# Kernel optimization log

Hardware: AMD Instinct MI355X
Metric: run time of the kernel (lower is better)

The kernel has to match this reference:

```python
import jax, jax.numpy as jnp
import numpy as np
import math

FEAT_DIM = 128
N_BANK = 1000000
K_NEG = 4096
BATCH = 256
T = 0.5
MOMENTUM = 0.5
EPS = 1e-7


def setup_inputs() -> dict:
    key = jax.random.key(0)
    k1, k2, k3, k4, k5, k6 = jax.random.split(key, 6)
    stdv = 1.0 / math.sqrt(FEAT_DIM / 3)
    memory_l = jax.random.uniform(k1, (N_BANK, FEAT_DIM), minval=-stdv, maxval=stdv, dtype=jnp.float32)
    memory_ab = jax.random.uniform(k2, (N_BANK, FEAT_DIM), minval=-stdv, maxval=stdv, dtype=jnp.float32)
    l = jax.random.normal(k3, (BATCH, FEAT_DIM), dtype=jnp.float32)
    ab = jax.random.normal(k4, (BATCH, FEAT_DIM), dtype=jnp.float32)
    y = jax.random.randint(k5, (BATCH,), 0, N_BANK, dtype=jnp.int32)
    idx = jax.random.randint(k6, (BATCH, K_NEG + 1), 0, N_BANK, dtype=jnp.int32)
    idx = idx.at[:, 0].set(y)  # positive sample in slot 0, as in torch forward
    return {"l": l, "ab": ab, "memory_l": memory_l, "memory_ab": memory_ab, "y": y, "idx": idx}


def _l2_normalize(x):
    # matches torch: x / (sqrt(sum(x^2)) + eps)
    return x / (jnp.sqrt(jnp.sum(x * x, axis=1, keepdims=True)) + EPS)


def _momentum_update(memory, y, x_norm):
    # gather rows, momentum mix, renormalize, scatter back
    pos = memory[y] * MOMENTUM + x_norm * (1.0 - MOMENTUM)          # [B, D]
    norm = jnp.sqrt(jnp.sum(pos * pos, axis=1, keepdims=True))
    return memory.at[y].set(pos / norm)


def reference(l, ab, memory_l, memory_ab, y, idx):
    outputSize = memory_l.shape[0]
    ln = _l2_normalize(l)
    abn = _l2_normalize(ab)

    # gather negatives+positive from the AB bank, score against l features
    w_ab = jax.lax.stop_gradient(memory_ab[idx])                     # [B, K+1, D]
    P_l = jnp.exp(jnp.einsum('bkd,bd->bk', w_ab, ln) / T)[..., None]  # [B, K+1, 1]
    Z_l = jnp.mean(P_l) * outputSize
    out_l = P_l / Z_l

    w_l = jax.lax.stop_gradient(memory_l[idx])                       # [B, K+1, D]
    P_ab = jnp.exp(jnp.einsum('bkd,bd->bk', w_l, abn) / T)[..., None]
    Z_ab = jnp.mean(P_ab) * outputSize
    out_ab = P_ab / Z_ab

    # momentum scatter update of the memory banks (no_grad in torch)
    new_memory_l = jax.lax.stop_gradient(_momentum_update(memory_l, y, ln))
    new_memory_ab = jax.lax.stop_gradient(_momentum_update(memory_ab, y, abn))

    return out_l, out_ab, new_memory_l, new_memory_ab
```

## Files before the change

### kernel.cpp

```cpp
#include <hip/hip_runtime.h>
#include <math.h>
#include <stdint.h>

#define FEAT   128
#define NBANK  1000000
#define KP1    4097
#define BATCH  256
#define INV_T  2.0f
#define EPS_N  1e-7f

constexpr size_t TOTP   = (size_t)BATCH * KP1;
constexpr size_t O_OUTL = 0;
constexpr size_t O_OUTA = TOTP;
constexpr size_t O_MEML = 2 * TOTP;
constexpr size_t O_MEMA = O_MEML + (size_t)NBANK * FEAT;

constexpr int RPB   = 16;
constexpr int NBUCK = NBANK / RPB;
constexpr int CAP   = 64;

constexpr int CHUNK  = 31;
constexpr int GRID_M = (NBUCK + CHUNK - 1) / CHUNK;

constexpr size_t WS_LN   = 0;
constexpr size_t WS_ABN  = 32768;
constexpr size_t WS_PL   = 65544;
constexpr size_t WS_PA   = 65800;
constexpr size_t WS_U32  = 66560;

typedef float vfloat4 __attribute__((ext_vector_type(4)));

__device__ __forceinline__ float dot4(vfloat4 a, vfloat4 b) {
    return a.x * b.x + a.y * b.y + a.z * b.z + a.w * b.w;
}

__global__ void norm_zero_kernel(const float* __restrict__ l,
                                 const float* __restrict__ ab,
                                 float* __restrict__ ws,
                                 unsigned int* __restrict__ cnt) {
    int b    = blockIdx.x;
    int lane = threadIdx.x;
    for (int i = b * 64 + lane; i < NBUCK; i += 512 * 64) cnt[i] = 0u;
    const float* src;
    float*       dst;
    if (b < BATCH) { src = l  + (size_t)b * FEAT;            dst = ws + WS_LN  + (size_t)b * FEAT; }
    else           { src = ab + (size_t)(b - BATCH) * FEAT;  dst = ws + WS_ABN + (size_t)(b - BATCH) * FEAT; }
    float2 v = *(const float2*)(src + 2 * lane);
    float  ss = v.x * v.x + v.y * v.y;
    #pragma unroll
    for (int m = 1; m < 64; m <<= 1) ss += __shfl_xor(ss, m, 64);
    float inv = 1.0f / (sqrtf(ss) + EPS_N);
    ((float2*)dst)[lane] = make_float2(v.x * inv, v.y * inv);
}

__global__ void build_kernel(const int* __restrict__ idx,
                             unsigned int* __restrict__ cnt,
                             unsigned int* __restrict__ ent) {
    size_t stride = (size_t)gridDim.x * blockDim.x;
    for (size_t p = (size_t)blockIdx.x * blockDim.x + threadIdx.x; p < TOTP; p += stride) {
        int row = idx[p];
        int b   = (int)(p / KP1);
        int k   = (int)(p - (size_t)b * KP1);
        int bucket = row >> 4;
        unsigned int pos = atomicAdd(&cnt[bucket], 1u);
        if (pos < (unsigned int)CAP)
            ent[(size_t)bucket * CAP + pos] =
                ((unsigned int)b << 17) | ((unsigned int)k << 4) | (unsigned int)(row & 15);
    }
}

__global__ __launch_bounds__(256) void main_kernel(
        const float* __restrict__ mem_l, const float* __restrict__ mem_ab,
        const float* __restrict__ ws_f,
        const unsigned int* __restrict__ cnt,
        const unsigned int* __restrict__ ent,
        float* __restrict__ out) {
    __shared__ float ldsL[RPB * FEAT];
    __shared__ float ldsA[RPB * FEAT];
    int tid = threadIdx.x;
    int w0  = blockIdx.x * CHUNK;
    int w1  = min(w0 + CHUNK, NBUCK);
    if (w0 >= NBUCK) return;

    vfloat4* lL = (vfloat4*)ldsL;
    vfloat4* lA = (vfloat4*)ldsA;
    int g = tid >> 4, lane16 = tid & 15;

    size_t fb = (size_t)w0 * RPB * FEAT;
    vfloat4 cl0 = ((const vfloat4*)(mem_l  + fb))[tid];
    vfloat4 cl1 = ((const vfloat4*)(mem_l  + fb))[256 + tid];
    vfloat4 ca0 = ((const vfloat4*)(mem_ab + fb))[tid];
    vfloat4 ca1 = ((const vfloat4*)(mem_ab + fb))[256 + tid];
    int c = min((int)cnt[w0], CAP);

    for (int w = w0; w < w1; ++w) {
        size_t fbase = (size_t)w * RPB * FEAT;
        lL[tid] = cl0; lL[256 + tid] = cl1;
        lA[tid] = ca0; lA[256 + tid] = ca1;
        ((vfloat4*)(out + O_MEML + fbase))[tid]       = cl0;
        ((vfloat4*)(out + O_MEML + fbase))[256 + tid] = cl1;
        ((vfloat4*)(out + O_MEMA + fbase))[tid]       = ca0;
        ((vfloat4*)(out + O_MEMA + fbase))[256 + tid] = ca1;
        vfloat4 nl0, nl1, na0, na1; int cn = 0;
        if (w + 1 < w1) {
            size_t nb = (size_t)(w + 1) * RPB * FEAT;
            nl0 = ((const vfloat4*)(mem_l  + nb))[tid];
            nl1 = ((const vfloat4*)(mem_l  + nb))[256 + tid];
            na0 = ((const vfloat4*)(mem_ab + nb))[tid];
            na1 = ((const vfloat4*)(mem_ab + nb))[256 + tid];
            cn  = min((int)cnt[w + 1], CAP);
        }
        asm volatile("s_waitcnt lgkmcnt(0)" ::: "memory");
        __builtin_amdgcn_s_barrier();
        for (int i = g; i < c; i += 16) {
            unsigned int ev = ent[(size_t)w * CAP + i];
            int rloc = (int)(ev & 15u);
            int k    = (int)((ev >> 4) & 0x1FFFu);
            int b    = (int)(ev >> 17);
            const vfloat4* ra = (const vfloat4*)(ldsA + rloc * FEAT) + lane16 * 2;
            const vfloat4* rl = (const vfloat4*)(ldsL + rloc * FEAT) + lane16 * 2;
            vfloat4 wa0 = ra[0], wa1 = ra[1];
            vfloat4 wl0 = rl[0], wl1 = rl[1];
            const vfloat4* lq = (const vfloat4*)(ws_f + WS_LN  + (size_t)b * FEAT) + lane16 * 2;
            const vfloat4* aq = (const vfloat4*)(ws_f + WS_ABN + (size_t)b * FEAT) + lane16 * 2;
            vfloat4 lv0 = lq[0], lv1 = lq[1];
            vfloat4 av0 = aq[0], av1 = aq[1];
            float dlv  = dot4(wa0, lv0) + dot4(wa1, lv1);
            float dabv = dot4(wl0, av0) + dot4(wl1, av1);
            #pragma unroll
            for (int m = 1; m < 16; m <<= 1) {
                dlv  += __shfl_xor(dlv,  m, 64);
                dabv += __shfl_xor(dabv, m, 64);
            }
            if (lane16 == 0) {
                out[O_OUTL + (size_t)b * KP1 + k] = __expf(dlv  * INV_T);
                out[O_OUTA + (size_t)b * KP1 + k] = __expf(dabv * INV_T);
            }
        }
        __builtin_amdgcn_s_barrier();
        cl0 = nl0; cl1 = nl1; ca0 = na0; ca1 = na1; c = cn;
    }
}

__global__ void zsum_kernel(const float* __restrict__ out,
                            float* __restrict__ pl, float* __restrict__ pa) {
    __shared__ float sl[256], sa[256];
    int i = blockIdx.x, t = threadIdx.x;
    const float* bl = out + O_OUTL + (size_t)i * KP1;
    const float* ba = out + O_OUTA + (size_t)i * KP1;
    float a = 0.f, b = 0.f;
    for (int p = t; p < KP1; p += 256) { a += bl[p]; b += ba[p]; }
    sl[t] = a; sa[t] = b;
    __syncthreads();
    for (int s = 128; s > 0; s >>= 1) {
        if (t < s) { sl[t] += sl[t + s]; sa[t] += sa[t + s]; }
        __syncthreads();
    }
    if (t == 0) { pl[i] = sl[0]; pa[i] = sa[0]; }
}

__global__ void finish_kernel(const float* __restrict__ pl,
                              const float* __restrict__ pa,
                              const float* __restrict__ mem_l,
                              const float* __restrict__ mem_ab,
                              const int*   __restrict__ y,
                              const float* __restrict__ ws,
                              float* __restrict__ out) {
    __shared__ float s2[2];
    int b = blockIdx.x, t = threadIdx.x;
    if (t == 0) {
        float a = 0.f, c = 0.f;
        for (int i = 0; i < 256; ++i) { a += pl[i]; c += pa[i]; }
        float count = (float)TOTP;
        s2[0] = count / (a * (float)NBANK);
        s2[1] = count / (c * (float)NBANK);
    }
    __syncthreads();
    float zl = s2[0], za = s2[1];
    float* bl = out + O_OUTL + (size_t)b * KP1;
    float* ba = out + O_OUTA + (size_t)b * KP1;
    for (int p = t; p < KP1; p += 256) { bl[p] *= zl; ba[p] *= za; }

    if (t < 64) {
        int lane = t;
        int row  = y[b];
        bool win = true;
        for (int j = b + 1; j < BATCH; ++j)
            if (y[j] == row) { win = false; break; }
        if (win) {
            {
                float2 m = ((const float2*)(mem_l + (size_t)row * FEAT))[lane];
                float2 x = ((const float2*)(ws + WS_LN + (size_t)b * FEAT))[lane];
                float2 p = make_float2(m.x * 0.5f + x.x * 0.5f, m.y * 0.5f + x.y * 0.5f);
                float ss = p.x * p.x + p.y * p.y;
                #pragma unroll
                for (int mk = 1; mk < 64; mk <<= 1) ss += __shfl_xor(ss, mk, 64);
                float nrm = sqrtf(ss);
                ((float2*)(out + O_MEML + (size_t)row * FEAT))[lane] =
                    make_float2(p.x / nrm, p.y / nrm);
            }
            {
                float2 m = ((const float2*)(mem_ab + (size_t)row * FEAT))[lane];
                float2 x = ((const float2*)(ws + WS_ABN + (size_t)b * FEAT))[lane];
                float2 p = make_float2(m.x * 0.5f + x.x * 0.5f, m.y * 0.5f + x.y * 0.5f);
                float ss = p.x * p.x + p.y * p.y;
                #pragma unroll
                for (int mk = 1; mk < 64; mk <<= 1) ss += __shfl_xor(ss, mk, 64);
                float nrm = sqrtf(ss);
                ((float2*)(out + O_MEMA + (size_t)row * FEAT))[lane] =
                    make_float2(p.x / nrm, p.y / nrm);
            }
        }
    }
}

extern "C" void kernel_launch(void* const* d_in, const int* in_sizes, int n_in,
                              void* d_out, int out_size, void* d_ws, size_t ws_size,
                              hipStream_t stream) {
    const float* l      = (const float*)d_in[0];
    const float* ab     = (const float*)d_in[1];
    const float* mem_l  = (const float*)d_in[2];
    const float* mem_ab = (const float*)d_in[3];
    const int*   y      = (const int*)d_in[4];
    const int*   idx    = (const int*)d_in[5];
    float* out = (float*)d_out;
    float* ws  = (float*)d_ws;

    unsigned int* wsu = (unsigned int*)(ws + WS_U32);
    unsigned int* cnt = wsu;
    unsigned int* ent = wsu + NBUCK;

    norm_zero_kernel<<<dim3(2 * BATCH), dim3(64), 0, stream>>>(l, ab, ws, cnt);
    build_kernel<<<dim3(2048), dim3(256), 0, stream>>>(idx, cnt, ent);
    main_kernel<<<dim3(GRID_M), dim3(256), 0, stream>>>(
        mem_l, mem_ab, ws, cnt, ent, out);
    zsum_kernel<<<dim3(256), dim3(256), 0, stream>>>(out, ws + WS_PL, ws + WS_PA);
    finish_kernel<<<dim3(BATCH), dim3(256), 0, stream>>>(
        ws + WS_PL, ws + WS_PA, mem_l, mem_ab, y, ws, out);
}
```

Baseline: 573.3 us.

## Double-buffer LDS bucket tiles and switch main kernel to grid-stride persistent blocks

The main kernel now runs as a fixed grid of 1024 persistent blocks that stride over buckets, replacing contiguous chunks of 31 buckets per block. LDS tiles are double-buffered, which removes the trailing barrier in each iteration, and a sched_barrier keeps the compiler from moving work across the wait and barrier. The aim is to cut per-iteration synchronisation and to even out load across CUs. In exchange, consecutive buckets handled by one block are no longer adjacent in memory, LDS use per block doubles, and the grid shrinks to 1024 blocks.

```diff
diff --git a/kernel.cpp b/kernel.cpp
--- a/kernel.cpp
+++ b/kernel.cpp
@@ -19,8 +19,7 @@
 constexpr int NBUCK = NBANK / RPB;
 constexpr int CAP   = 64;
 
-constexpr int CHUNK  = 31;
-constexpr int GRID_M = (NBUCK + CHUNK - 1) / CHUNK;
+constexpr int GRID_M = 1024;
 
 constexpr size_t WS_LN   = 0;
 constexpr size_t WS_ABN  = 32768;
@@ -75,50 +74,52 @@
         const unsigned int* __restrict__ cnt,
         const unsigned int* __restrict__ ent,
         float* __restrict__ out) {
-    __shared__ float ldsL[RPB * FEAT];
-    __shared__ float ldsA[RPB * FEAT];
+    __shared__ float ldsL[2][RPB * FEAT];
+    __shared__ float ldsA[2][RPB * FEAT];
     int tid = threadIdx.x;
-    int w0  = blockIdx.x * CHUNK;
-    int w1  = min(w0 + CHUNK, NBUCK);
-    if (w0 >= NBUCK) return;
-
-    vfloat4* lL = (vfloat4*)ldsL;
-    vfloat4* lA = (vfloat4*)ldsA;
     int g = tid >> 4, lane16 = tid & 15;
 
-    size_t fb = (size_t)w0 * RPB * FEAT;
+    int w = blockIdx.x;
+    size_t fb = (size_t)w * RPB * FEAT;
     vfloat4 cl0 = ((const vfloat4*)(mem_l  + fb))[tid];
     vfloat4 cl1 = ((const vfloat4*)(mem_l  + fb))[256 + tid];
     vfloat4 ca0 = ((const vfloat4*)(mem_ab + fb))[tid];
     vfloat4 ca1 = ((const vfloat4*)(mem_ab + fb))[256 + tid];
-    int c = min((int)cnt[w0], CAP);
-
-    for (int w = w0; w < w1; ++w) {
+    int c = min((int)cnt[w], CAP);
+
+    int buf = 0;
+    for (;;) {
         size_t fbase = (size_t)w * RPB * FEAT;
-        lL[tid] = cl0; lL[256 + tid] = cl1;
-        lA[tid] = ca0; lA[256 + tid] = ca1;
+        ((vfloat4*)ldsL[buf])[tid]       = cl0;
+        ((vfloat4*)ldsL[buf])[256 + tid] = cl1;
+        ((vfloat4*)ldsA[buf])[tid]       = ca0;
+        ((vfloat4*)ldsA[buf])[256 + tid] = ca1;
         ((vfloat4*)(out + O_MEML + fbase))[tid]       = cl0;
         ((vfloat4*)(out + O_MEML + fbase))[256 + tid] = cl1;
         ((vfloat4*)(out + O_MEMA + fbase))[tid]       = ca0;
         ((vfloat4*)(out + O_MEMA + fbase))[256 + tid] = ca1;
+        int wn = w + GRID_M;
         vfloat4 nl0, nl1, na0, na1; int cn = 0;
-        if (w + 1 < w1) {
-            size_t nb = (size_t)(w + 1) * RPB * FEAT;
+        if (wn < NBUCK) {
+            size_t nb = (size_t)wn * RPB * FEAT;
             nl0 = ((const vfloat4*)(mem_l  + nb))[tid];
             nl1 = ((const vfloat4*)(mem_l  + nb))[256 + tid];
             na0 = ((const vfloat4*)(mem_ab + nb))[tid];
             na1 = ((const vfloat4*)(mem_ab + nb))[256 + tid];
-            cn  = min((int)cnt[w + 1], CAP);
+            cn  = min((int)cnt[wn], CAP);
         }
         asm volatile("s_waitcnt lgkmcnt(0)" ::: "memory");
+        __builtin_amdgcn_sched_barrier(0);
         __builtin_amdgcn_s_barrier();
+        const float* bL = ldsL[buf];
+        const float* bA = ldsA[buf];
         for (int i = g; i < c; i += 16) {
             unsigned int ev = ent[(size_t)w * CAP + i];
             int rloc = (int)(ev & 15u);
             int k    = (int)((ev >> 4) & 0x1FFFu);
             int b    = (int)(ev >> 17);
-            const vfloat4* ra = (const vfloat4*)(ldsA + rloc * FEAT) + lane16 * 2;
-            const vfloat4* rl = (const vfloat4*)(ldsL + rloc * FEAT) + lane16 * 2;
+            const vfloat4* ra = (const vfloat4*)(bA + rloc * FEAT) + lane16 * 2;
+            const vfloat4* rl = (const vfloat4*)(bL + rloc * FEAT) + lane16 * 2;
             vfloat4 wa0 = ra[0], wa1 = ra[1];
             vfloat4 wl0 = rl[0], wl1 = rl[1];
             const vfloat4* lq = (const vfloat4*)(ws_f + WS_LN  + (size_t)b * FEAT) + lane16 * 2;
@@ -137,8 +138,9 @@
                 out[O_OUTA + (size_t)b * KP1 + k] = __expf(dabv * INV_T);
             }
         }
-        __builtin_amdgcn_s_barrier();
-        cl0 = nl0; cl1 = nl1; ca0 = na0; ca1 = na1; c = cn;
+        if (wn >= NBUCK) break;
+        w = wn; cl0 = nl0; cl1 = nl1; ca0 = na0; ca1 = na1; c = cn;
+        buf ^= 1;
     }
 }
 
```

New measurement: 533.3 us. 7.0% less time.

## Launch one block per bucket instead of chunked loop with register prefetch

Applied to the files above, without the earlier changes.

Replaces the persistent-style main kernel, where each block walks 31 buckets with software prefetch of the next bucket, with one block per 16-row bucket (62500 blocks). Bucket entries are staged into shared memory before scoring. This relies on the hardware scheduler and many resident blocks to hide memory latency instead of manual double-buffering, at the cost of more block launch overhead and no explicit overlap within a block.

```diff
diff --git a/kernel.cpp b/kernel.cpp
--- a/kernel.cpp
+++ b/kernel.cpp
@@ -18,9 +18,6 @@
 constexpr int RPB   = 16;
 constexpr int NBUCK = NBANK / RPB;
 constexpr int CAP   = 64;
-
-constexpr int CHUNK  = 31;
-constexpr int GRID_M = (NBUCK + CHUNK - 1) / CHUNK;
 
 constexpr size_t WS_LN   = 0;
 constexpr size_t WS_ABN  = 32768;
@@ -77,68 +74,58 @@
         float* __restrict__ out) {
     __shared__ float ldsL[RPB * FEAT];
     __shared__ float ldsA[RPB * FEAT];
+    __shared__ unsigned int sEnt[CAP];
+    int blk = blockIdx.x;
     int tid = threadIdx.x;
-    int w0  = blockIdx.x * CHUNK;
-    int w1  = min(w0 + CHUNK, NBUCK);
-    if (w0 >= NBUCK) return;
+    size_t fbase = (size_t)blk * RPB * FEAT;
+
+    int c = min((int)cnt[blk], CAP);
+    if (tid < CAP && tid < c) sEnt[tid] = ent[(size_t)blk * CAP + tid];
+
+    const vfloat4* sl = (const vfloat4*)(mem_l  + fbase);
+    const vfloat4* sa = (const vfloat4*)(mem_ab + fbase);
+    vfloat4 vl[2], va[2];
+    #pragma unroll
+    for (int j = 0; j < 2; ++j) vl[j] = sl[j * 256 + tid];
+    #pragma unroll
+    for (int j = 0; j < 2; ++j) va[j] = sa[j * 256 + tid];
 
     vfloat4* lL = (vfloat4*)ldsL;
     vfloat4* lA = (vfloat4*)ldsA;
+    #pragma unroll
+    for (int j = 0; j < 2; ++j) { int i = j * 256 + tid; lL[i] = vl[j]; lA[i] = va[j]; }
+    __syncthreads();
+
+    vfloat4* dl_ = (vfloat4*)(out + O_MEML + fbase);
+    vfloat4* da_ = (vfloat4*)(out + O_MEMA + fbase);
+    #pragma unroll
+    for (int j = 0; j < 2; ++j) { int i = j * 256 + tid; dl_[i] = vl[j]; da_[i] = va[j]; }
+
     int g = tid >> 4, lane16 = tid & 15;
-
-    size_t fb = (size_t)w0 * RPB * FEAT;
-    vfloat4 cl0 = ((const vfloat4*)(mem_l  + fb))[tid];
-    vfloat4 cl1 = ((const vfloat4*)(mem_l  + fb))[256 + tid];
-    vfloat4 ca0 = ((const vfloat4*)(mem_ab + fb))[tid];
-    vfloat4 ca1 = ((const vfloat4*)(mem_ab + fb))[256 + tid];
-    int c = min((int)cnt[w0], CAP);
-
-    for (int w = w0; w < w1; ++w) {
-        size_t fbase = (size_t)w * RPB * FEAT;
-        lL[tid] = cl0; lL[256 + tid] = cl1;
-        lA[tid] = ca0; lA[256 + tid] = ca1;
-        ((vfloat4*)(out + O_MEML + fbase))[tid]       = cl0;
-        ((vfloat4*)(out + O_MEML + fbase))[256 + tid] = cl1;
-        ((vfloat4*)(out + O_MEMA + fbase))[tid]       = ca0;
-        ((vfloat4*)(out + O_MEMA + fbase))[256 + tid] = ca1;
-        vfloat4 nl0, nl1, na0, na1; int cn = 0;
-        if (w + 1 < w1) {
-            size_t nb = (size_t)(w + 1) * RPB * FEAT;
-            nl0 = ((const vfloat4*)(mem_l  + nb))[tid];
-            nl1 = ((const vfloat4*)(mem_l  + nb))[256 + tid];
-            na0 = ((const vfloat4*)(mem_ab + nb))[tid];
-            na1 = ((const vfloat4*)(mem_ab + nb))[256 + tid];
-            cn  = min((int)cnt[w + 1], CAP);
+    for (int i = g; i < c; i += 16) {
+        unsigned int ev = sEnt[i];
+        int rloc = (int)(ev & 15u);
+        int k    = (int)((ev >> 4) & 0x1FFFu);
+        int b    = (int)(ev >> 17);
+        const vfloat4* ra = (const vfloat4*)(ldsA + rloc * FEAT) + lane16 * 2;
+        const vfloat4* rl = (const vfloat4*)(ldsL + rloc * FEAT) + lane16 * 2;
+        vfloat4 wa0 = ra[0], wa1 = ra[1];
+        vfloat4 wl0 = rl[0], wl1 = rl[1];
+        const vfloat4* lq = (const vfloat4*)(ws_f + WS_LN  + (size_t)b * FEAT) + lane16 * 2;
+        const vfloat4* aq = (const vfloat4*)(ws_f + WS_ABN + (size_t)b * FEAT) + lane16 * 2;
+        vfloat4 lv0 = lq[0], lv1 = lq[1];
+        vfloat4 av0 = aq[0], av1 = aq[1];
+        float dlv  = dot4(wa0, lv0) + dot4(wa1, lv1);
+        float dabv = dot4(wl0, av0) + dot4(wl1, av1);
+        #pragma unroll
+        for (int m = 1; m < 16; m <<= 1) {
+            dlv  += __shfl_xor(dlv,  m, 64);
+            dabv += __shfl_xor(dabv, m, 64);
         }
-        asm volatile("s_waitcnt lgkmcnt(0)" ::: "memory");
-        __builtin_amdgcn_s_barrier();
-        for (int i = g; i < c; i += 16) {
-            unsigned int ev = ent[(size_t)w * CAP + i];
-            int rloc = (int)(ev & 15u);
-            int k    = (int)((ev >> 4) & 0x1FFFu);
-            int b    = (int)(ev >> 17);
-            const vfloat4* ra = (const vfloat4*)(ldsA + rloc * FEAT) + lane16 * 2;
-            const vfloat4* rl = (const vfloat4*)(ldsL + rloc * FEAT) + lane16 * 2;
-            vfloat4 wa0 = ra[0], wa1 = ra[1];
-            vfloat4 wl0 = rl[0], wl1 = rl[1];
-            const vfloat4* lq = (const vfloat4*)(ws_f + WS_LN  + (size_t)b * FEAT) + lane16 * 2;
-            const vfloat4* aq = (const vfloat4*)(ws_f + WS_ABN + (size_t)b * FEAT) + lane16 * 2;
-            vfloat4 lv0 = lq[0], lv1 = lq[1];
-            vfloat4 av0 = aq[0], av1 = aq[1];
-            float dlv  = dot4(wa0, lv0) + dot4(wa1, lv1);
-            float dabv = dot4(wl0, av0) + dot4(wl1, av1);
-            #pragma unroll
-            for (int m = 1; m < 16; m <<= 1) {
-                dlv  += __shfl_xor(dlv,  m, 64);
-                dabv += __shfl_xor(dabv, m, 64);
-            }
-            if (lane16 == 0) {
-                out[O_OUTL + (size_t)b * KP1 + k] = __expf(dlv  * INV_T);
-                out[O_OUTA + (size_t)b * KP1 + k] = __expf(dabv * INV_T);
-            }
+        if (lane16 == 0) {
+            out[O_OUTL + (size_t)b * KP1 + k] = __expf(dlv  * INV_T);
+            out[O_OUTA + (size_t)b * KP1 + k] = __expf(dabv * INV_T);
         }
-        __builtin_amdgcn_s_barrier();
-        cl0 = nl0; cl1 = nl1; ca0 = na0; ca1 = na1; c = cn;
     }
 }
 
@@ -232,7 +219,7 @@
 
     norm_zero_kernel<<<dim3(2 * BATCH), dim3(64), 0, stream>>>(l, ab, ws, cnt);
     build_kernel<<<dim3(2048), dim3(256), 0, stream>>>(idx, cnt, ent);
-    main_kernel<<<dim3(GRID_M), dim3(256), 0, stream>>>(
+    main_kernel<<<dim3(NBUCK), dim3(256), 0, stream>>>(
         mem_l, mem_ab, ws, cnt, ent, out);
     zsum_kernel<<<dim3(256), dim3(256), 0, stream>>>(out, ws + WS_PL, ws + WS_PA);
     finish_kernel<<<dim3(BATCH), dim3(256), 0, stream>>>(
```

After: 486.4 us. 1.18x faster.
